# Performance work log

Measured on AMD Instinct MI355X. Metric: run time of the kernel, lower is better.

## Reference

```python
import jax, jax.numpy as jnp
import numpy as np

N = 100000
E = 800000
IN_CH = 128
HID = 32
HEADS = 8
OUT_CH = 40
NEG_SLOPE = 0.2


def setup_inputs() -> dict:
    key = jax.random.key(0)
    ks = jax.random.split(key, 10)
    x = jax.random.normal(ks[0], (N, IN_CH), dtype=jnp.float32)
    edge_index = jax.random.randint(ks[1], (2, E), 0, N, dtype=jnp.int64)
    # GATConv layer 1: in -> heads*hid, concat=True
    s1 = 1.0 / np.sqrt(IN_CH)
    W1 = jax.random.uniform(ks[2], (IN_CH, HEADS * HID), jnp.float32, -s1, s1)
    att_src1 = jax.random.uniform(ks[3], (1, HEADS, HID), jnp.float32, -s1, s1)
    att_dst1 = jax.random.uniform(ks[4], (1, HEADS, HID), jnp.float32, -s1, s1)
    b1 = jnp.zeros((HEADS * HID,), jnp.float32)
    # GATConv layer 2: heads*hid -> out, heads=1, concat=True
    s2 = 1.0 / np.sqrt(HEADS * HID)
    W2 = jax.random.uniform(ks[5], (HEADS * HID, OUT_CH), jnp.float32, -s2, s2)
    att_src2 = jax.random.uniform(ks[6], (1, 1, OUT_CH), jnp.float32, -s2, s2)
    att_dst2 = jax.random.uniform(ks[7], (1, 1, OUT_CH), jnp.float32, -s2, s2)
    b2 = jnp.zeros((OUT_CH,), jnp.float32)
    return {"x": x, "edge_index": edge_index,
            "W1": W1, "att_src1": att_src1, "att_dst1": att_dst1, "b1": b1,
            "W2": W2, "att_src2": att_src2, "att_dst2": att_dst2, "b2": b2}


def _gat_layer(x, src, dst, W, att_src, att_dst, bias, heads, out_ch):
    n = x.shape[0]
    xp = (x @ W).reshape(n, heads, out_ch)               # [N,H,C]
    a_src = jnp.sum(xp * att_src, axis=-1)               # [N,H]
    a_dst = jnp.sum(xp * att_dst, axis=-1)               # [N,H]
    logits = a_src[src] + a_dst[dst]                      # [Etot,H]
    logits = jnp.where(logits > 0, logits, NEG_SLOPE * logits)  # leaky_relu
    # segment softmax over destination node
    m = jax.ops.segment_max(logits, dst, num_segments=n)  # [N,H]
    p = jnp.exp(logits - m[dst])
    z = jax.ops.segment_sum(p, dst, num_segments=n)
    alpha = p / (z[dst] + 1e-16)                           # [Etot,H]
    out = jax.ops.segment_sum(xp[src] * alpha[:, :, None], dst, num_segments=n)
    return out.reshape(n, heads * out_ch) + bias


def reference(x, edge_index, W1, att_src1, att_dst1, b1, W2, att_src2, att_dst2, b2):
    n = x.shape[0]
    # add self loops (PyG GATConv default add_self_loops=True)
    loop = jnp.arange(n, dtype=edge_index.dtype)
    src = jnp.concatenate([edge_index[0], loop])
    dst = jnp.concatenate([edge_index[1], loop])
    # dropout p=0.2 is identity in eval mode
    h = _gat_layer(x, src, dst, W1, att_src1, att_dst1, b1, HEADS, HID)
    h = jax.nn.relu(h)
    out = _gat_layer(h, src, dst, W2, att_src2, att_dst2, b2, 1, OUT_CH)
    return jax.nn.log_softmax(out, axis=1)
```

## Files before the change

### kernel.cpp

```cpp
#include <hip/hip_runtime.h>
#include <math.h>

#define NN 100000
#define NE 800000
#define C1 256
#define OC 40
#define XPAD 64
#define NEG 0.2f
#define FCHUNK 4096
#define G1BLK 782

typedef _Float16 h4 __attribute__((ext_vector_type(4)));
typedef _Float16 h8 __attribute__((ext_vector_type(8)));
typedef float f4v __attribute__((ext_vector_type(4)));
typedef float f2v __attribute__((ext_vector_type(2)));

static __device__ __forceinline__ float leaky(float v){ return v > 0.f ? v : NEG*v; }

static __device__ __forceinline__ h8 mk8(float4 a, float4 b){
  h8 r = {(_Float16)a.x,(_Float16)a.y,(_Float16)a.z,(_Float16)a.w,
          (_Float16)b.x,(_Float16)b.y,(_Float16)b.z,(_Float16)b.w};
  return r;
}

static __device__ __forceinline__ void gload_lds16h(const _Float16* g, _Float16* l){
  __builtin_amdgcn_global_load_lds((const __attribute__((address_space(1))) void*)g,
                                   (__attribute__((address_space(3))) void*)l, 16, 0, 0);
}


__global__ __launch_bounds__(256) void k_wt(const float* __restrict__ W1, const float* __restrict__ W2,
                                            const float* __restrict__ aS1, const float* __restrict__ aD1,
                                            const float* __restrict__ aS2, const float* __restrict__ aD2,
                                            _Float16* __restrict__ W1s, _Float16* __restrict__ W2t,
                                            int* __restrict__ deg){
  int b = blockIdx.x;
  if (b < 128){
    int k = b, c = threadIdx.x;
    W1s[(size_t)c*128 + (((k>>3) ^ (c&15))<<3) + (k&7)] = (_Float16)W1[k*256 + c];
  } else if (b < 176){
    int nb = b - 128;
    int e = threadIdx.x;
    int l = e >> 2, j = e & 3;
    int k = (l>>5)*128 + ((l>>4)&1)*64 + j*16 + (l&15);
    float v = (nb < OC) ? W2[(size_t)k*OC + nb] : 0.f;
    W2t[(size_t)nb*256 + e] = (_Float16)v;
  } else if (b < 178){
    int b2 = b - 176;
    int h  = threadIdx.x >> 5;
    int kb = (threadIdx.x & 31) * 4;
    const float* att = b2 ? aD1 : aS1;
    const int c = 256 + b2*8 + h;
    #pragma unroll
    for (int kk = 0; kk < 4; ++kk){
      int k = kb + kk;
      float s = 0.f;
      for (int cc = 0; cc < 32; ++cc) s += W1[k*256 + h*32 + cc] * att[h*32 + cc];
      W1s[(size_t)c*128 + (((k>>3) ^ (c&15))<<3) + (k&7)] = (_Float16)s;
    }
  } else if (b < 194){
    int j = b - 178;
    int e = threadIdx.x;
    int l = e >> 2, jj = e & 3;
    int k = (l>>5)*128 + ((l>>4)&1)*64 + jj*16 + (l&15);
    float v = 0.f;
    if (j == 0){ for (int c = 0; c < OC; ++c) v += W2[(size_t)k*OC + c] * aS2[c]; }
    else if (j == 1){ for (int c = 0; c < OC; ++c) v += W2[(size_t)k*OC + c] * aD2[c]; }
    W2t[(size_t)(48 + j)*256 + e] = (_Float16)v;
  } else {
    int i = (b - 194)*256 + threadIdx.x;
    if (i < NN) deg[i] = 1;
  }
}

__global__ __launch_bounds__(512, 4) void k_gemm1(const float* __restrict__ x,
    const _Float16* __restrict__ W1s, unsigned* __restrict__ xp1w,
    float* __restrict__ asrc, float* __restrict__ adst,
    const int* __restrict__ ei, int* __restrict__ deg)
{
  __shared__ _Float16 bs[272*128];
  if (blockIdx.x >= G1BLK){
    int i = (blockIdx.x - G1BLK)*512 + threadIdx.x;
    if (i < NE) atomicAdd(&deg[ei[NE + i]], 1);
    return;
  }
  const int tid  = threadIdx.x;
  const int lane = tid & 63;
  const int w    = tid >> 6;
  const int n = lane & 15, quad = lane >> 4;
  const int r0 = blockIdx.x * 128 + w*16;

  #pragma unroll
  for (int it = 0; it < 8; ++it){
    int idx = it*512 + tid;
    gload_lds16h(W1s + (size_t)idx*8, bs + (size_t)(it*512 + w*64)*8);
  }
  if (w < 4){
    int idx = 4096 + w*64 + lane;
    gload_lds16h(W1s + (size_t)idx*8, bs + (size_t)(4096 + w*64)*8);
  }

  int ra = r0 + n; ra = ra < NN ? ra : NN-1;
  const float* xr = x + (size_t)ra*128 + quad*8;
  float4 fa[4][2];
  #pragma unroll
  for (int ks = 0; ks < 4; ++ks){
    fa[ks][0] = *(const float4*)(xr + ks*32);
    fa[ks][1] = *(const float4*)(xr + ks*32 + 4);
  }

  __syncthreads();

  f4v acc[17];
  #pragma unroll
  for (int ct = 0; ct < 17; ++ct) acc[ct] = (f4v){0.f,0.f,0.f,0.f};

  #pragma unroll
  for (int ks = 0; ks < 4; ++ks){
    h8 a = mk8(fa[ks][0], fa[ks][1]);
    #pragma unroll
    for (int ct = 0; ct < 17; ++ct){
      const int col = ct*16 + n;
      h8 b = *((const h8*)bs + (size_t)col*16 + (((ks*4 + quad) ^ n)));
      acc[ct] = __builtin_amdgcn_mfma_f32_16x16x32_f16(a, b, acc[ct], 0, 0, 0);
    }
  }

  #pragma unroll
  for (int reg = 0; reg < 4; ++reg){
    const int row = r0 + quad*4 + reg;
    if (row < NN){
      float v[16];
      #pragma unroll
      for (int ct = 0; ct < 16; ++ct) v[ct] = acc[ct][reg];
      unsigned dw0 = (unsigned)__builtin_amdgcn_cvt_pk_fp8_f32(v[0], v[1], 0, false);
      dw0 = (unsigned)__builtin_amdgcn_cvt_pk_fp8_f32(v[2], v[3], (int)dw0, true);
      unsigned dw1 = (unsigned)__builtin_amdgcn_cvt_pk_fp8_f32(v[4], v[5], 0, false);
      dw1 = (unsigned)__builtin_amdgcn_cvt_pk_fp8_f32(v[6], v[7], (int)dw1, true);
      unsigned dw2 = (unsigned)__builtin_amdgcn_cvt_pk_fp8_f32(v[8], v[9], 0, false);
      dw2 = (unsigned)__builtin_amdgcn_cvt_pk_fp8_f32(v[10], v[11], (int)dw2, true);
      unsigned dw3 = (unsigned)__builtin_amdgcn_cvt_pk_fp8_f32(v[12], v[13], 0, false);
      dw3 = (unsigned)__builtin_amdgcn_cvt_pk_fp8_f32(v[14], v[15], (int)dw3, true);
      unsigned* xw = xp1w + (size_t)row*64;
      xw[n]      = dw0;
      xw[16 + n] = dw1;
      xw[32 + n] = dw2;
      xw[48 + n] = dw3;
      float vE = acc[16][reg];
      if (n < 8) asrc[row*8 + n] = vE;
      else       adst[row*8 + (n - 8)] = vE;
    }
  }
}

__global__ __launch_bounds__(256) void k_scan1(const int* __restrict__ deg, int* part, int* bsum){
  __shared__ int lds[256];
  const int t = threadIdx.x;
  const int base = blockIdx.x*1024;
  int v[4]; int s = 0;
  #pragma unroll
  for (int i = 0; i < 4; ++i){ int idx = base + t*4 + i; v[i] = (idx < NN) ? deg[idx] : 0; s += v[i]; }
  lds[t] = s; __syncthreads();
  for (int off = 1; off < 256; off <<= 1){
    int xx = (t >= off) ? lds[t-off] : 0;
    __syncthreads();
    lds[t] += xx;
    __syncthreads();
  }
  int excl = lds[t] - s;
  #pragma unroll
  for (int i = 0; i < 4; ++i){ int idx = base + t*4 + i; if (idx < NN) part[idx] = excl; excl += v[i]; }
  if (t == 255) bsum[blockIdx.x] = lds[255];
}
__global__ void k_scan2(const int* __restrict__ bsum, int* boff){
  const int l = threadIdx.x;
  int a = (l      < 98) ? bsum[l]      : 0;
  int b = (64 + l < 98) ? bsum[64 + l] : 0;
  int sa = a, sb = b;
  #pragma unroll
  for (int off = 1; off < 64; off <<= 1){
    int ta = __shfl_up(sa, off, 64);
    int tb = __shfl_up(sb, off, 64);
    if (l >= off){ sa += ta; sb += tb; }
  }
  const int totalA = __shfl(sa, 63, 64);
  if (l      < 98) boff[l]      = sa - a;
  if (64 + l < 98) boff[64 + l] = totalA + sb - b;
}
__global__ __launch_bounds__(256) void k_scan3(const int* __restrict__ part, const int* __restrict__ boff,
                                               int* rowptr, int* cursor){
  int i = blockIdx.x*256 + threadIdx.x;
  if (i < NN){ int v = part[i] + boff[i >> 10]; rowptr[i] = v; cursor[i] = v; }
  if (i == 0) rowptr[NN] = NN + NE;
}
__global__ __launch_bounds__(256) void k_fill(const int* __restrict__ ei, int* cursor, int* __restrict__ esrc){
  const int xcd = blockIdx.x & 7;
  const int base = (blockIdx.x >> 3) * FCHUNK;
  const int lo = xcd * (NN/8), hi = lo + (NN/8);
  const int end = (base + FCHUNK < NE + NN) ? (base + FCHUNK) : (NE + NN);
  for (int i = base + threadIdx.x; i < end; i += 256){
    int s, d;
    if (i < NE){ s = ei[i]; d = ei[NE + i]; } else { s = d = i - NE; }
    if (d >= lo && d < hi){
      int slot = atomicAdd(&cursor[d], 1);
      esrc[slot] = s;
    }
  }
}

template<int B>
static __device__ __forceinline__ void agg1_batch(
    const int j0, const int je, const int lane,
    const int* __restrict__ esrc, const float* __restrict__ asrc,
    const float adA, const float adB,
    const unsigned* __restrict__ xp1w,
    f2v& accLo, f2v& accHi, float& z0, float& z1)
{
  const int cnt = je - j0;
  const int slot = lane & 15;
  const int hA = (lane >> 4) << 1;
  int idx = j0 + slot; idx = idx < je ? idx : je - 1;
  const int sv = esrc[idx];
  float pv0 = 0.f, pv1 = 0.f;
  if (slot < cnt){
    f2v av = *(const f2v*)(asrc + (size_t)sv*8 + hA);
    pv0 = __expf(leaky(av.x + adA));
    pv1 = __expf(leaky(av.y + adB));
  }
  z0 += pv0; z1 += pv1;
  unsigned u[B];
  #pragma unroll
  for (int e = 0; e < B; ++e){
    int s = __builtin_amdgcn_readlane(sv, e);
    u[e] = xp1w[(size_t)s*64 + lane];
  }
  __builtin_amdgcn_sched_barrier(0);
  const int pb = lane & 48;
  #pragma unroll
  for (int e = 0; e < B; ++e){
    const float pA = __shfl(pv0, pb | e, 64);
    const float pB = __shfl(pv1, pb | e, 64);
    f2v lo = __builtin_amdgcn_cvt_pk_f32_fp8((int)u[e], false);
    f2v hi = __builtin_amdgcn_cvt_pk_f32_fp8((int)u[e], true);
    accLo += (f2v){pA, pA} * lo;
    accHi += (f2v){pB, pB} * hi;
  }
}

__global__ __launch_bounds__(256) void k_agg1(const unsigned* __restrict__ xp1w,
    const float* __restrict__ asrc, const float* __restrict__ adst,
    const float* __restrict__ b1, const int* __restrict__ rowptr,
    const int* __restrict__ esrc, _Float16* __restrict__ h1)
{
  const int lane = threadIdx.x & 63;
  int n = __builtin_amdgcn_readfirstlane(blockIdx.x*4 + (threadIdx.x >> 6));
  const int hA = (lane >> 4) << 1;
  const f2v ad = *(const f2v*)(adst + (size_t)n*8 + hA);
  const int jb = rowptr[n], je = rowptr[n+1];
  const int cbase = (lane>>5)*128 + ((lane>>4)&1)*64 + (lane&15);
  const float bp0 = b1[cbase], bp1 = b1[cbase+16], bp2 = b1[cbase+32], bp3 = b1[cbase+48];
  f2v accLo = {0.f,0.f}, accHi = {0.f,0.f};
  float z0 = 0.f, z1 = 0.f;

  int j0 = jb;
  while (j0 < je){
    if (je - j0 > 8){
      agg1_batch<16>(j0, je, lane, esrc, asrc, ad.x, ad.y, xp1w, accLo, accHi, z0, z1);
      j0 += 16;
    } else {
      agg1_batch<8>(j0, je, lane, esrc, asrc, ad.x, ad.y, xp1w, accLo, accHi, z0, z1);
      j0 += 8;
    }
  }
  #pragma unroll
  for (int off = 1; off <= 8; off <<= 1){
    z0 += __shfl_xor(z0, off, 64);
    z1 += __shfl_xor(z1, off, 64);
  }
  const float invA = 1.f/(z0 + 1e-16f), invB = 1.f/(z1 + 1e-16f);
  h4 o = {(_Float16)fmaxf(accLo.x*invA + bp0, 0.f),
          (_Float16)fmaxf(accLo.y*invA + bp1, 0.f),
          (_Float16)fmaxf(accHi.x*invB + bp2, 0.f),
          (_Float16)fmaxf(accHi.y*invB + bp3, 0.f)};
  ((h4*)h1)[(size_t)n*64 + lane] = o;
}

__global__ __launch_bounds__(256) void k_gemm2(const _Float16* __restrict__ h1,
    const _Float16* __restrict__ W2t, _Float16* __restrict__ xp2,
    float* __restrict__ asrc2, float* __restrict__ adst2)
{
  const int tid  = threadIdx.x;
  const int lane = tid & 63;
  const int w    = tid >> 6;
  const int n = lane & 15, quad = lane >> 4;
  const int r0 = blockIdx.x * 64 + w*16;

  f4v acc[4];
  #pragma unroll
  for (int ct = 0; ct < 4; ++ct) acc[ct] = (f4v){0.f,0.f,0.f,0.f};

  int rr = r0 + n; rr = rr < NN ? rr : NN-1;

  #pragma unroll
  for (int ks = 0; ks < 8; ++ks){
    h8 a = *(const h8*)(h1 + (size_t)rr*256 + ks*32 + quad*8);
    #pragma unroll
    for (int ct = 0; ct < 4; ++ct){
      h8 b = *(const h8*)(W2t + (size_t)(ct*16 + n)*256 + ks*32 + quad*8);
      acc[ct] = __builtin_amdgcn_mfma_f32_16x16x32_f16(a, b, acc[ct], 0, 0, 0);
    }
  }

  #pragma unroll
  for (int reg = 0; reg < 4; ++reg){
    const int row = r0 + quad*4 + reg;
    if (row < NN){
      float v0 = acc[0][reg], v1 = acc[1][reg], v2 = acc[2][reg], v3 = acc[3][reg];
      _Float16* xr = xp2 + (size_t)row*XPAD + n;
      xr[0]  = (_Float16)v0;
      xr[16] = (_Float16)v1;
      if (n < 8) xr[32] = (_Float16)v2;
      if (n == 0) asrc2[row] = v3;
      if (n == 1) adst2[row] = v3;
    }
  }
}

__global__ __launch_bounds__(256) void k_agg2(const _Float16* __restrict__ xp2,
    const float* __restrict__ asrc2, const float* __restrict__ adst2,
    const float* __restrict__ b2, const int* __restrict__ rowptr,
    const int* __restrict__ esrc, float* __restrict__ out)
{
  const int lane = threadIdx.x & 63;
  const int g = lane >> 4;
  const int t = lane & 15;
  int n = __builtin_amdgcn_readfirstlane(blockIdx.x*4 + (threadIdx.x >> 6));
  const float ad = adst2[n];
  const int jb = rowptr[n], je = rowptr[n+1];
  f4v acc = {0.f,0.f,0.f,0.f};
  float zacc = 0.f;

  for (int j0 = jb; j0 < je; j0 += 16){
    const int cnt = je - j0;
    int idx = j0 + t; idx = idx < je ? idx : je - 1;
    const int sv = esrc[idx];
    const float pv = (t < cnt) ? __expf(leaky(asrc2[sv] + ad)) : 0.f;
    zacc += pv;
    h4 u[4];
    #pragma unroll
    for (int e4 = 0; e4 < 4; ++e4){
      int svg = __shfl(sv, e4*4 + g, 64);
      u[e4] = *(const h4*)(xp2 + (size_t)svg*XPAD + t*4);
    }
    __builtin_amdgcn_sched_barrier(0);
    #pragma unroll
    for (int e4 = 0; e4 < 4; ++e4){
      const float p = __shfl(pv, e4*4 + g, 64);
      acc.x += p*(float)u[e4].x;
      acc.y += p*(float)u[e4].y;
      acc.z += p*(float)u[e4].z;
      acc.w += p*(float)u[e4].w;
    }
  }
  #pragma unroll
  for (int off = 1; off <= 8; off <<= 1) zacc += __shfl_xor(zacc, off, 64);
  #pragma unroll
  for (int off = 16; off <= 32; off <<= 1){
    acc.x += __shfl_xor(acc.x, off, 64);
    acc.y += __shfl_xor(acc.y, off, 64);
    acc.z += __shfl_xor(acc.z, off, 64);
    acc.w += __shfl_xor(acc.w, off, 64);
  }
  const float inv = 1.f/(zacc + 1e-16f);
  const bool act = t < 10;
  float4 bv = act ? *(const float4*)(b2 + 4*t) : make_float4(0.f,0.f,0.f,0.f);
  float v0 = acc.x*inv + bv.x, v1 = acc.y*inv + bv.y;
  float v2 = acc.z*inv + bv.z, v3 = acc.w*inv + bv.w;
  float m = act ? fmaxf(fmaxf(v0,v1), fmaxf(v2,v3)) : -INFINITY;
  #pragma unroll
  for (int off = 1; off <= 8; off <<= 1) m = fmaxf(m, __shfl_xor(m, off, 64));
  float es = act ? (__expf(v0-m)+__expf(v1-m)+__expf(v2-m)+__expf(v3-m)) : 0.f;
  #pragma unroll
  for (int off = 1; off <= 8; off <<= 1) es += __shfl_xor(es, off, 64);
  if (lane < 10){
    float lse = m + __logf(es);
    float4 o = make_float4(v0-lse, v1-lse, v2-lse, v3-lse);
    *(float4*)(out + (size_t)n*OC + 4*t) = o;
  }
}

extern "C" void kernel_launch(void* const* d_in, const int* in_sizes, int n_in,
                              void* d_out, int out_size, void* d_ws, size_t ws_size,
                              hipStream_t stream)
{
  const float* x   = (const float*)d_in[0];
  const int*   ei  = (const int*)  d_in[1];
  const float* W1  = (const float*)d_in[2];
  const float* aS1 = (const float*)d_in[3];
  const float* aD1 = (const float*)d_in[4];
  const float* b1  = (const float*)d_in[5];
  const float* W2  = (const float*)d_in[6];
  const float* aS2 = (const float*)d_in[7];
  const float* aD2 = (const float*)d_in[8];
  const float* b2  = (const float*)d_in[9];
  float* out = (float*)d_out;

  char* wsp = (char*)d_ws;
  size_t off = 0;
  auto alloc = [&](size_t bytes){ void* p = wsp + off; off += (bytes + 255) & ~(size_t)255; return p; };
  unsigned* xp1w = (unsigned*)alloc((size_t)NN*C1);
  _Float16* h1  = (_Float16*)alloc((size_t)NN*C1*2);
  float* as1  = (float*)alloc((size_t)NN*8*4);
  float* ad1  = (float*)alloc((size_t)NN*8*4);
  float* as2  = (float*)alloc((size_t)NN*4);
  float* ad2  = (float*)alloc((size_t)NN*4);
  int* deg    = (int*)alloc((size_t)NN*4);
  int* part   = (int*)alloc((size_t)NN*4);
  int* rowptr = (int*)alloc((size_t)(NN+1)*4);
  int* cursor = (int*)alloc((size_t)NN*4);
  int* bsum   = (int*)alloc(98*4);
  int* boff   = (int*)alloc(98*4);
  int* esrc   = (int*)alloc((size_t)(NN+NE)*4);
  _Float16* W1s = (_Float16*)alloc((size_t)272*128*2);
  _Float16* W2t = (_Float16*)alloc((size_t)64*256*2);
  _Float16* xp2 = (_Float16*)alloc((size_t)NN*XPAD*2);
  (void)ws_size; (void)in_sizes; (void)n_in; (void)out_size;

  const int fill_chunks = (NE + NN + FCHUNK - 1) / FCHUNK;
  const int deg_blocks  = (NE + 511) / 512;

  k_wt    <<<194 + (NN + 255)/256, 256, 0, stream>>>(W1, W2, aS1, aD1, aS2, aD2, W1s, W2t, deg);
  k_gemm1 <<<G1BLK + deg_blocks,   512, 0, stream>>>(x, W1s, xp1w, as1, ad1, ei, deg);
  k_scan1 <<<98,   256, 0, stream>>>(deg, part, bsum);
  k_scan2 <<<1,    64,  0, stream>>>(bsum, boff);
  k_scan3 <<<391,  256, 0, stream>>>(part, boff, rowptr, cursor);
  k_fill  <<<fill_chunks*8, 256, 0, stream>>>(ei, cursor, esrc);
  k_agg1  <<<25000,256, 0, stream>>>(xp1w, as1, ad1, b1, rowptr, esrc, h1);
  k_gemm2 <<<1563, 256, 0, stream>>>(h1, W2t, xp2, as2, ad2);
  k_agg2  <<<25000,256, 0, stream>>>(xp2, as2, ad2, b2, rowptr, esrc, out);
}
```

Baseline: 322.7 us.

## Fuse layer-2 projection GEMM into layer-1 aggregation via shared memory

The layer-1 aggregation kernel now runs 16 waves per block, one destination node each, and stages the ReLU'd hidden rows in LDS. Four of those waves then compute the 256x64 projection with MFMA, writing xp2 and the layer-2 attention scalars directly. This drops the 51 MB fp16 h1 round trip through global memory and one kernel launch. In exchange it adds a block-wide barrier, so the slowest node's edge loop (degree imbalance) idles the other 15 waves. The 1024-thread blocks may also lower occupancy.

```diff
diff --git a/kernel.cpp b/kernel.cpp
--- a/kernel.cpp
+++ b/kernel.cpp
@@ -247,13 +247,16 @@
   }
 }
 
-__global__ __launch_bounds__(256) void k_agg1(const unsigned* __restrict__ xp1w,
+__global__ __launch_bounds__(1024) void k_agg1(const unsigned* __restrict__ xp1w,
     const float* __restrict__ asrc, const float* __restrict__ adst,
     const float* __restrict__ b1, const int* __restrict__ rowptr,
-    const int* __restrict__ esrc, _Float16* __restrict__ h1)
+    const int* __restrict__ esrc, const _Float16* __restrict__ W2t,
+    _Float16* __restrict__ xp2, float* __restrict__ asrc2, float* __restrict__ adst2)
 {
+  __shared__ _Float16 hs[16*264];
   const int lane = threadIdx.x & 63;
-  int n = __builtin_amdgcn_readfirstlane(blockIdx.x*4 + (threadIdx.x >> 6));
+  const int w = threadIdx.x >> 6;
+  int n = __builtin_amdgcn_readfirstlane(blockIdx.x*16 + w);
   const int hA = (lane >> 4) << 1;
   const f2v ad = *(const f2v*)(adst + (size_t)n*8 + hA);
   const int jb = rowptr[n], je = rowptr[n+1];
@@ -282,46 +285,29 @@
           (_Float16)fmaxf(accLo.y*invA + bp1, 0.f),
           (_Float16)fmaxf(accHi.x*invB + bp2, 0.f),
           (_Float16)fmaxf(accHi.y*invB + bp3, 0.f)};
-  ((h4*)h1)[(size_t)n*64 + lane] = o;
-}
-
-__global__ __launch_bounds__(256) void k_gemm2(const _Float16* __restrict__ h1,
-    const _Float16* __restrict__ W2t, _Float16* __restrict__ xp2,
-    float* __restrict__ asrc2, float* __restrict__ adst2)
-{
-  const int tid  = threadIdx.x;
-  const int lane = tid & 63;
-  const int w    = tid >> 6;
-  const int n = lane & 15, quad = lane >> 4;
-  const int r0 = blockIdx.x * 64 + w*16;
-
-  f4v acc[4];
-  #pragma unroll
-  for (int ct = 0; ct < 4; ++ct) acc[ct] = (f4v){0.f,0.f,0.f,0.f};
-
-  int rr = r0 + n; rr = rr < NN ? rr : NN-1;
-
-  #pragma unroll
-  for (int ks = 0; ks < 8; ++ks){
-    h8 a = *(const h8*)(h1 + (size_t)rr*256 + ks*32 + quad*8);
-    #pragma unroll
-    for (int ct = 0; ct < 4; ++ct){
-      h8 b = *(const h8*)(W2t + (size_t)(ct*16 + n)*256 + ks*32 + quad*8);
-      acc[ct] = __builtin_amdgcn_mfma_f32_16x16x32_f16(a, b, acc[ct], 0, 0, 0);
-    }
-  }
-
-  #pragma unroll
-  for (int reg = 0; reg < 4; ++reg){
-    const int row = r0 + quad*4 + reg;
-    if (row < NN){
-      float v0 = acc[0][reg], v1 = acc[1][reg], v2 = acc[2][reg], v3 = acc[3][reg];
-      _Float16* xr = xp2 + (size_t)row*XPAD + n;
-      xr[0]  = (_Float16)v0;
-      xr[16] = (_Float16)v1;
-      if (n < 8) xr[32] = (_Float16)v2;
-      if (n == 0) asrc2[row] = v3;
-      if (n == 1) adst2[row] = v3;
+  ((h4*)(hs + (size_t)w*264))[lane] = o;
+
+  __syncthreads();
+
+  if (w < 4){
+    const int nq = lane & 15, quad = lane >> 4;
+    f4v acc = (f4v){0.f,0.f,0.f,0.f};
+    #pragma unroll
+    for (int ks = 0; ks < 8; ++ks){
+      h8 a = *(const h8*)(hs + (size_t)nq*264 + ks*32 + quad*8);
+      h8 b = *(const h8*)(W2t + (size_t)(w*16 + nq)*256 + ks*32 + quad*8);
+      acc = __builtin_amdgcn_mfma_f32_16x16x32_f16(a, b, acc, 0, 0, 0);
+    }
+    const int nb = __builtin_amdgcn_readfirstlane(blockIdx.x*16);
+    #pragma unroll
+    for (int reg = 0; reg < 4; ++reg){
+      const int row = nb + quad*4 + reg;
+      float v = acc[reg];
+      _Float16* xr = xp2 + (size_t)row*XPAD;
+      if (w == 0)      xr[nq]      = (_Float16)v;
+      else if (w == 1) xr[16 + nq] = (_Float16)v;
+      else if (w == 2){ if (nq < 8) xr[32 + nq] = (_Float16)v; }
+      else { if (nq == 0) asrc2[row] = v; else if (nq == 1) adst2[row] = v; }
     }
   }
 }
@@ -409,7 +395,6 @@
   size_t off = 0;
   auto alloc = [&](size_t bytes){ void* p = wsp + off; off += (bytes + 255) & ~(size_t)255; return p; };
   unsigned* xp1w = (unsigned*)alloc((size_t)NN*C1);
-  _Float16* h1  = (_Float16*)alloc((size_t)NN*C1*2);
   float* as1  = (float*)alloc((size_t)NN*8*4);
   float* ad1  = (float*)alloc((size_t)NN*8*4);
   float* as2  = (float*)alloc((size_t)NN*4);
@@ -435,7 +420,6 @@
   k_scan2 <<<1,    64,  0, stream>>>(bsum, boff);
   k_scan3 <<<391,  256, 0, stream>>>(part, boff, rowptr, cursor);
   k_fill  <<<fill_chunks*8, 256, 0, stream>>>(ei, cursor, esrc);
-  k_agg1  <<<25000,256, 0, stream>>>(xp1w, as1, ad1, b1, rowptr, esrc, h1);
-  k_gemm2 <<<1563, 256, 0, stream>>>(h1, W2t, xp2, as2, ad2);
+  k_agg1  <<<6250, 1024, 0, stream>>>(xp1w, as1, ad1, b1, rowptr, esrc, W2t, xp2, as2, ad2);
   k_agg2  <<<25000,256, 0, stream>>>(xp2, as2, ad2, b2, rowptr, esrc, out);
 }
```

After: 308.5 us. -4.4%, faster.
